# Kernel tuning notes

Hardware: AMD Instinct MI355X
Metric: run time of the kernel (lower is better)

## Reference

```python
import jax, jax.numpy as jnp
import numpy as np
from jax import lax

T, B, NI, NH = 512, 64, 512, 512
SIGMA = 0.01


def _rnn_scan(inputs, W_xh, W_hh, b_h, h0):
    # inputs: [T, B, NI]; precompute input projection as one big GEMM
    xw = jnp.einsum('tbi,ih->tbh', inputs, W_xh)  # [T, B, NH]

    def step(h, x):
        h = jnp.tanh(x + h @ W_hh + b_h)
        return h, h

    hT, hs = lax.scan(step, h0, xw)
    return hs, hT  # hs: [T, B, NH]


def setup_inputs() -> dict:
    key = jax.random.key(0)
    ks = jax.random.split(key, 5)
    inputs = jax.random.normal(ks[0], (T, B, NI), dtype=jnp.float32)
    W_xh_f = jax.random.normal(ks[1], (NI, NH), dtype=jnp.float32) * SIGMA
    W_hh_f = jax.random.normal(ks[2], (NH, NH), dtype=jnp.float32) * SIGMA
    b_h_f = jnp.zeros((NH,), dtype=jnp.float32)
    W_xh_b = jax.random.normal(ks[3], (NI, NH), dtype=jnp.float32) * SIGMA
    W_hh_b = jax.random.normal(ks[4], (NH, NH), dtype=jnp.float32) * SIGMA
    b_h_b = jnp.zeros((NH,), dtype=jnp.float32)
    return {"inputs": inputs, "W_xh_f": W_xh_f, "W_hh_f": W_hh_f, "b_h_f": b_h_f,
            "W_xh_b": W_xh_b, "W_hh_b": W_hh_b, "b_h_b": b_h_b}


def reference(inputs, W_xh_f, W_hh_f, b_h_f, W_xh_b, W_hh_b, b_h_b):
    h0 = jnp.zeros((inputs.shape[1], NH), dtype=inputs.dtype)
    f_outs, f_H = _rnn_scan(inputs, W_xh_f, W_hh_f, b_h_f, h0)
    b_outs_rev, b_H = _rnn_scan(inputs[::-1], W_xh_b, W_hh_b, b_h_b, h0)
    b_outs = b_outs_rev[::-1]  # align backward outputs with forward time order
    outputs = jnp.concatenate([f_outs, b_outs], axis=-1)  # [T, B, 2*NH]
    return outputs, f_H, b_H
```

## Files before the change

kernel.cpp:

```cpp
#include <hip/hip_runtime.h>
#include <hip/hip_bf16.h>


typedef __attribute__((ext_vector_type(8))) short short8;
typedef __attribute__((ext_vector_type(4))) float f32x4;
typedef __attribute__((ext_vector_type(4))) int   i32x4;

static __device__ __forceinline__ float bf2f(unsigned short s) {
  return __builtin_bit_cast(float, ((unsigned int)s) << 16);
}
static __device__ __forceinline__ float tanh_cheap(float x) {
  float t = x * 2.8853900817779268f;
  float e;
  asm("v_exp_f32 %0, %1" : "=v"(e) : "v"(t));
  float den = e + 1.0f;
  float r;
  asm("v_rcp_f32 %0, %1" : "=v"(r) : "v"(den));
  return __builtin_fmaf(-2.0f, r, 1.0f);
}
static __device__ __forceinline__ void lds_barrier() {
  __builtin_amdgcn_sched_barrier(0);
  asm volatile("s_waitcnt lgkmcnt(0)" ::: "memory");
  __builtin_amdgcn_s_barrier();
  __builtin_amdgcn_sched_barrier(0);
}
static __device__ __forceinline__ unsigned int cvt_pk_bf16(float a, float b) {
  unsigned int d;
  asm("v_cvt_pk_bf16_f32 %0, %1, %2" : "=v"(d) : "v"(a), "v"(b));
  return d;
}

__global__ __launch_bounds__(256, 4) void xw_gemm(
    const float* __restrict__ inp,
    const float* __restrict__ Wf,
    const float* __restrict__ Wb,
    const float* __restrict__ bhf,
    const float* __restrict__ bhb,
    unsigned short* __restrict__ xwpf,
    unsigned short* __restrict__ xwpb) {
  __shared__ __align__(16) unsigned short As[64 * 40];
  __shared__ __align__(16) unsigned short Bfs[64 * 40];
  __shared__ __align__(16) unsigned short Bbs[64 * 40];
  const int tid = threadIdx.x;
  const int w = tid >> 6, l = tid & 63;
  const int lr = l & 15, lg = l >> 4;
  const int rbase = blockIdx.x * 64;
  const int nbase = blockIdx.y * 64;

  f32x4 accf[4], accb[4];
#pragma unroll
  for (int tn = 0; tn < 4; ++tn) { accf[tn] = (f32x4){0,0,0,0}; accb[tn] = (f32x4){0,0,0,0}; }

  for (int i = 0; i < 16; ++i) {
    const int k0 = i * 32;
    __syncthreads();
#pragma unroll
    for (int e = 0; e < 2; ++e) {
      int lin4 = tid + e * 256;
      int r = lin4 >> 3, c4 = (lin4 & 7) * 4;
      float4 v = *reinterpret_cast<const float4*>(&inp[(rbase + r) * 512 + k0 + c4]);
      uint2 p;
      p.x = cvt_pk_bf16(v.x, v.y);
      p.y = cvt_pk_bf16(v.z, v.w);
      *reinterpret_cast<uint2*>(&As[r * 40 + c4]) = p;
    }
#pragma unroll
    for (int e = 0; e < 2; ++e) {
      int lin4 = tid + e * 256;
      int r = lin4 >> 4, c4 = (lin4 & 15) * 4;
      float4 vf = *reinterpret_cast<const float4*>(&Wf[(k0 + r) * 512 + nbase + c4]);
      float4 vb = *reinterpret_cast<const float4*>(&Wb[(k0 + r) * 512 + nbase + c4]);
      unsigned int uf0 = cvt_pk_bf16(vf.x, vf.y);
      unsigned int uf1 = cvt_pk_bf16(vf.z, vf.w);
      unsigned int ub0 = cvt_pk_bf16(vb.x, vb.y);
      unsigned int ub1 = cvt_pk_bf16(vb.z, vb.w);
      Bfs[(c4 + 0) * 40 + r] = (unsigned short)uf0;
      Bfs[(c4 + 1) * 40 + r] = (unsigned short)(uf0 >> 16);
      Bfs[(c4 + 2) * 40 + r] = (unsigned short)uf1;
      Bfs[(c4 + 3) * 40 + r] = (unsigned short)(uf1 >> 16);
      Bbs[(c4 + 0) * 40 + r] = (unsigned short)ub0;
      Bbs[(c4 + 1) * 40 + r] = (unsigned short)(ub0 >> 16);
      Bbs[(c4 + 2) * 40 + r] = (unsigned short)ub1;
      Bbs[(c4 + 3) * 40 + r] = (unsigned short)(ub1 >> 16);
    }
    __syncthreads();
    const int ar = w * 16 + lr;
    const int kg = lg * 8;
    short8 a = *reinterpret_cast<const short8*>(&As[ar * 40 + kg]);
#pragma unroll
    for (int tn = 0; tn < 4; ++tn) {
      const int bc = tn * 16 + lr;
      short8 bf = *reinterpret_cast<const short8*>(&Bfs[bc * 40 + kg]);
      short8 bb = *reinterpret_cast<const short8*>(&Bbs[bc * 40 + kg]);
      accf[tn] = __builtin_amdgcn_mfma_f32_16x16x32_bf16(a, bf, accf[tn], 0, 0, 0);
      accb[tn] = __builtin_amdgcn_mfma_f32_16x16x32_bf16(a, bb, accb[tn], 0, 0, 0);
    }
  }
  unsigned long long* pf = reinterpret_cast<unsigned long long*>(xwpf);
  unsigned long long* pb = reinterpret_cast<unsigned long long*>(xwpb);
  const int b64 = (((int)blockIdx.x * 4 + w) * 16 + (int)blockIdx.y * 2) * 128 +
                  (lg * 16 + lr) * 2;
#pragma unroll
  for (int tn = 0; tn < 4; ++tn) {
    const int colb = nbase + tn * 16 + lr;
    const float bfv = bhf[colb], bbv = bhb[colb];
    unsigned long long vf =
        (unsigned long long)cvt_pk_bf16(accf[tn][0] + bfv, accf[tn][1] + bfv)
      | ((unsigned long long)cvt_pk_bf16(accf[tn][2] + bfv, accf[tn][3] + bfv) << 32);
    unsigned long long vb =
        (unsigned long long)cvt_pk_bf16(accb[tn][0] + bbv, accb[tn][1] + bbv)
      | ((unsigned long long)cvt_pk_bf16(accb[tn][2] + bbv, accb[tn][3] + bbv) << 32);
    pf[b64 + (tn >> 1) * 128 + (tn & 1)] = vf;
    pb[b64 + (tn >> 1) * 128 + (tn & 1)] = vb;
  }
}

__global__ __launch_bounds__(1024) void birnn_scan(
    const float* __restrict__ Whf, const float* __restrict__ Whb,
    unsigned short* __restrict__ xwpf, unsigned short* __restrict__ xwpb,
    float* __restrict__ out) {
  const int bid = blockIdx.x;
  const int d  = bid >> 2;
  const int rg = bid & 3;
  const int tid = threadIdx.x;
  const int w = tid >> 6, l = tid & 63;
  const int lr = l & 15, lg = l >> 4;
  const int cbase = w * 32;
  const int rbase = rg * 16;

  const float* Wh = d ? Whb : Whf;
  unsigned short* xwp = d ? xwpb : xwpf;

  __shared__ __align__(16) signed char hq[2][8192];

  const float sW = 127.0f / 0.06f;
  i32x4 wq[2][8];
#pragma unroll
  for (int n = 0; n < 2; ++n) {
    const int col = cbase + n * 16 + lr;
#pragma unroll
    for (int kk = 0; kk < 8; ++kk) {
      i32x4 v;
#pragma unroll
      for (int dw = 0; dw < 4; ++dw) {
        unsigned int pack = 0;
#pragma unroll
        for (int jj = 0; jj < 4; ++jj) {
          const int k = kk * 64 + lg * 16 + dw * 4 + jj;
          float wv = Wh[k * 512 + col] * sW;
          wv = fminf(fmaxf(wv, -127.f), 127.f);
          int q = (int)rintf(wv);
          pack |= ((unsigned int)(q & 0xff)) << (8 * jj);
        }
        v[dw] = (int)pack;
      }
      wq[n][kk] = v;
    }
  }
  const float inv_s = 1.0f / (127.0f * sW);

  short8 xA, xB;
  {
    const int t0 = d ? 511 : 0;
    xA = *reinterpret_cast<const short8*>(
        xwp + (((t0 * 4 + rg) * 16 + w) << 9) + (l << 3));
  }
  {
    const int t1 = d ? 510 : 1;
    xB = *reinterpret_cast<const short8*>(
        xwp + (((t1 * 4 + rg) * 16 + w) << 9) + (l << 3));
  }

  uint4 HP;

#define EPI(N, ACC, U0, U1, FINAL_)                                           \
  {                                                                           \
    float h0_ = tanh_cheap(fmaf((float)(ACC)[0], inv_s, bf2f((unsigned short)X[(N)*4+0]))); \
    float h1_ = tanh_cheap(fmaf((float)(ACC)[1], inv_s, bf2f((unsigned short)X[(N)*4+1]))); \
    float h2_ = tanh_cheap(fmaf((float)(ACC)[2], inv_s, bf2f((unsigned short)X[(N)*4+2]))); \
    float h3_ = tanh_cheap(fmaf((float)(ACC)[3], inv_s, bf2f((unsigned short)X[(N)*4+3]))); \
    signed char* hd_ = &hq[buf_][(w * 2 + (N)) * 256 + lg * 64 + lr];         \
    hd_[0]  = (signed char)(int)rintf(h0_ * 127.f);                           \
    hd_[16] = (signed char)(int)rintf(h1_ * 127.f);                           \
    hd_[32] = (signed char)(int)rintf(h2_ * 127.f);                           \
    hd_[48] = (signed char)(int)rintf(h3_ * 127.f);                           \
    U0 = cvt_pk_bf16(h0_, h1_);                                               \
    U1 = cvt_pk_bf16(h2_, h3_);                                               \
    if (FINAL_) {                                                             \
      float* fo_ = out + 33554432 + d * 32768 + (rbase + lg * 4) * 512 +      \
                   cbase + (N) * 16 + lr;                                     \
      fo_[0] = h0_; fo_[512] = h1_; fo_[1024] = h2_; fo_[1536] = h3_;         \
    }                                                                         \
  }

#define STEP(S, XARG, FINAL_)                                                 \
  do {                                                                        \
    const int s_ = (S);                                                       \
    const int t_ = d ? (511 - s_) : s_;                                       \
    const int buf_ = s_ & 1;                                                  \
    const int pb_ = (s_ - 1) & 1;                                             \
    short8& X = (XARG);                                                       \
    {              \
      const int tp_ = d ? (t_ + 1) : (t_ - 1);                                \
      unsigned short* pw_ = xwp + (((tp_ * 4 + rg) * 16 + w) << 9) + (l << 3);\
      *reinterpret_cast<uint4*>(pw_) = HP;                                    \
    }                                                                         \
    i32x4 acc0 = (i32x4){0,0,0,0}, acc1 = (i32x4){0,0,0,0};                   \
    __builtin_amdgcn_s_setprio(1);                                            \
    {                        \
      const signed char* hb_ = &hq[pb_][lg * 256 + lr * 16];                  \
      i32x4 a0 = *(const i32x4*)(hb_ + 0);                                    \
      i32x4 a1 = *(const i32x4*)(hb_ + 1024);                                 \
      i32x4 a2 = *(const i32x4*)(hb_ + 2048);                                 \
      i32x4 a3 = *(const i32x4*)(hb_ + 3072);                                 \
      acc0 = __builtin_amdgcn_mfma_i32_16x16x64_i8(a0, wq[0][0], acc0, 0, 0, 0); \
      acc1 = __builtin_amdgcn_mfma_i32_16x16x64_i8(a0, wq[1][0], acc1, 0, 0, 0); \
      acc0 = __builtin_amdgcn_mfma_i32_16x16x64_i8(a1, wq[0][1], acc0, 0, 0, 0); \
      acc1 = __builtin_amdgcn_mfma_i32_16x16x64_i8(a1, wq[1][1], acc1, 0, 0, 0); \
      acc0 = __builtin_amdgcn_mfma_i32_16x16x64_i8(a2, wq[0][2], acc0, 0, 0, 0); \
      acc1 = __builtin_amdgcn_mfma_i32_16x16x64_i8(a2, wq[1][2], acc1, 0, 0, 0); \
      acc0 = __builtin_amdgcn_mfma_i32_16x16x64_i8(a3, wq[0][3], acc0, 0, 0, 0); \
      acc1 = __builtin_amdgcn_mfma_i32_16x16x64_i8(a3, wq[1][3], acc1, 0, 0, 0); \
    }                                                                         \
    {                                              \
      const signed char* hb_ = &hq[pb_][(16 + lg) * 256 + lr * 16];           \
      i32x4 a0 = *(const i32x4*)(hb_ + 0);                                    \
      i32x4 a1 = *(const i32x4*)(hb_ + 1024);                                 \
      i32x4 a2 = *(const i32x4*)(hb_ + 2048);                                 \
      i32x4 a3 = *(const i32x4*)(hb_ + 3072);                                 \
      acc0 = __builtin_amdgcn_mfma_i32_16x16x64_i8(a0, wq[0][4], acc0, 0, 0, 0); \
      acc1 = __builtin_amdgcn_mfma_i32_16x16x64_i8(a0, wq[1][4], acc1, 0, 0, 0); \
      acc0 = __builtin_amdgcn_mfma_i32_16x16x64_i8(a1, wq[0][5], acc0, 0, 0, 0); \
      acc1 = __builtin_amdgcn_mfma_i32_16x16x64_i8(a1, wq[1][5], acc1, 0, 0, 0); \
      acc0 = __builtin_amdgcn_mfma_i32_16x16x64_i8(a2, wq[0][6], acc0, 0, 0, 0); \
      acc1 = __builtin_amdgcn_mfma_i32_16x16x64_i8(a2, wq[1][6], acc1, 0, 0, 0); \
      acc0 = __builtin_amdgcn_mfma_i32_16x16x64_i8(a3, wq[0][7], acc0, 0, 0, 0); \
      acc1 = __builtin_amdgcn_mfma_i32_16x16x64_i8(a3, wq[1][7], acc1, 0, 0, 0); \
    }                                                                         \
    __builtin_amdgcn_s_setprio(0);                                            \
    EPI(0, acc0, HP.x, HP.y, FINAL_);                                         \
    EPI(1, acc1, HP.z, HP.w, FINAL_);                                         \
    {                                    \
      const int tp2_ = d ? (t_ - 2) : (t_ + 2);                               \
      X = *reinterpret_cast<const short8*>(                                   \
          xwp + (((tp2_ * 4 + rg) * 16 + w) << 9) + (l << 3));                \
    }                                                                         \
    lds_barrier();                                                            \
  } while (0)

  {
    const int t_ = d ? 511 : 0;
    const int buf_ = 0;
    short8& X = xA;
    i32x4 z_ = (i32x4){0, 0, 0, 0};
    EPI(0, z_, HP.x, HP.y, 0);
    EPI(1, z_, HP.z, HP.w, 0);
    {
      const int tp2_ = d ? (t_ - 2) : (t_ + 2);
      xA = *reinterpret_cast<const short8*>(
          xwp + (((tp2_ * 4 + rg) * 16 + w) << 9) + (l << 3));
    }
    lds_barrier();
  }

  for (int ss = 0; ss < 255; ++ss) {
    STEP(1 + 2 * ss, xB, 0);
    STEP(2 + 2 * ss, xA, 0);
  }
  STEP(511, xB, 1);

  {
    const int tl_ = d ? 0 : 511;
    unsigned short* pw_ = xwp + (((tl_ * 4 + rg) * 16 + w) << 9) + (l << 3);
    *reinterpret_cast<uint4*>(pw_) = HP;
  }
#undef STEP
#undef EPI
}

__global__ __launch_bounds__(1024) void expand_out(
    const unsigned short* __restrict__ xwpf,
    const unsigned short* __restrict__ xwpb,
    float* __restrict__ out) {
  const int g = blockIdx.x * 1024 + threadIdx.x;
  const int flat = g * 4;
  const int row = flat >> 10;
  const int c   = flat & 1023;
  const int t = row >> 6, b = row & 63;
  const int d = c >> 9, col = c & 511;
  const unsigned short* buf = d ? xwpb : xwpf;
  const int lr0 = col & 15;
  const int base = ((t * 4 + (b >> 4)) * 16 + (col >> 5)) * 512 +
                   (((b >> 2) & 3) * 16) * 8 + ((col >> 4) & 1) * 4 + (b & 3);
  float4 v;
  v.x = bf2f(buf[base + (lr0 + 0) * 8]);
  v.y = bf2f(buf[base + (lr0 + 1) * 8]);
  v.z = bf2f(buf[base + (lr0 + 2) * 8]);
  v.w = bf2f(buf[base + (lr0 + 3) * 8]);
  *reinterpret_cast<float4*>(out + flat) = v;
}

extern "C" void kernel_launch(void* const* d_in, const int* in_sizes, int n_in,
                              void* d_out, int out_size, void* d_ws, size_t ws_size,
                              hipStream_t stream) {
  (void)in_sizes; (void)n_in; (void)out_size; (void)ws_size;
  const float* inputs = (const float*)d_in[0];
  const float* W_xh_f = (const float*)d_in[1];
  const float* W_hh_f = (const float*)d_in[2];
  const float* b_h_f  = (const float*)d_in[3];
  const float* W_xh_b = (const float*)d_in[4];
  const float* W_hh_b = (const float*)d_in[5];
  const float* b_h_b  = (const float*)d_in[6];

  unsigned short* xwpf = (unsigned short*)d_ws;
  unsigned short* xwpb = xwpf + 16777216 + 65536;

  dim3 g1(512, 8), b1(256);
  xw_gemm<<<g1, b1, 0, stream>>>(inputs, W_xh_f, W_xh_b, b_h_f, b_h_b, xwpf, xwpb);

  birnn_scan<<<dim3(8), dim3(1024), 0, stream>>>(
      W_hh_f, W_hh_b, xwpf, xwpb, (float*)d_out);

  expand_out<<<dim3(8192), dim3(1024), 0, stream>>>(xwpf, xwpb, (float*)d_out);
}
```

Before: 847.6 us.

## Transpose scan MFMA operands so outputs are row-contiguous, swizzle hidden-state LDS

The recurrent int8 MFMA now takes the weights as the A operand and the hidden state as B, so each lane holds four consecutive hidden columns of one batch row. This lets the epilogue write packed 32-bit int8 hidden-state stores into an XOR-swizzled LDS layout, emit float4 final-state stores, and lets expand_out read one 64-bit word instead of four scattered 16-bit loads. The xw GEMM epilogue stages results through a new LDS tile so its output matches the new per-lane layout. This adds an extra LDS round trip and barriers in the GEMM, and the layout must stay consistent across all three kernels.

```diff
diff --git a/kernel.cpp b/kernel.cpp
--- a/kernel.cpp
+++ b/kernel.cpp
@@ -41,6 +41,7 @@
   __shared__ __align__(16) unsigned short As[64 * 40];
   __shared__ __align__(16) unsigned short Bfs[64 * 40];
   __shared__ __align__(16) unsigned short Bbs[64 * 40];
+  __shared__ __align__(16) unsigned short CT[2][64][68];
   const int tid = threadIdx.x;
   const int w = tid >> 6, l = tid & 63;
   const int lr = l & 15, lg = l >> 4;
@@ -96,22 +97,38 @@
       accb[tn] = __builtin_amdgcn_mfma_f32_16x16x32_bf16(a, bb, accb[tn], 0, 0, 0);
     }
   }
-  unsigned long long* pf = reinterpret_cast<unsigned long long*>(xwpf);
-  unsigned long long* pb = reinterpret_cast<unsigned long long*>(xwpb);
-  const int b64 = (((int)blockIdx.x * 4 + w) * 16 + (int)blockIdx.y * 2) * 128 +
-                  (lg * 16 + lr) * 2;
+  __syncthreads();
 #pragma unroll
   for (int tn = 0; tn < 4; ++tn) {
     const int colb = nbase + tn * 16 + lr;
     const float bfv = bhf[colb], bbv = bhb[colb];
-    unsigned long long vf =
-        (unsigned long long)cvt_pk_bf16(accf[tn][0] + bfv, accf[tn][1] + bfv)
-      | ((unsigned long long)cvt_pk_bf16(accf[tn][2] + bfv, accf[tn][3] + bfv) << 32);
-    unsigned long long vb =
-        (unsigned long long)cvt_pk_bf16(accb[tn][0] + bbv, accb[tn][1] + bbv)
-      | ((unsigned long long)cvt_pk_bf16(accb[tn][2] + bbv, accb[tn][3] + bbv) << 32);
-    pf[b64 + (tn >> 1) * 128 + (tn & 1)] = vf;
-    pb[b64 + (tn >> 1) * 128 + (tn & 1)] = vb;
+    const int gc = tn * 16 + lr;
+#pragma unroll
+    for (int q = 0; q < 4; ++q) {
+      const int gr = w * 16 + lg * 4 + q;
+      CT[0][gr][gc] = (unsigned short)cvt_pk_bf16(accf[tn][q] + bfv, 0.f);
+      CT[1][gr][gc] = (unsigned short)cvt_pk_bf16(accb[tn][q] + bbv, 0.f);
+    }
+  }
+  __syncthreads();
+  unsigned long long* const mats[2] = {
+      reinterpret_cast<unsigned long long*>(xwpf),
+      reinterpret_cast<unsigned long long*>(xwpb)};
+  const int idx0 = tid * 4;
+  const int rgl = idx0 >> 8;
+  const int wl  = (idx0 >> 7) & 1;
+  const int s0  = idx0 & 127;
+#pragma unroll
+  for (int m = 0; m < 2; ++m) {
+    unsigned long long* dst = mats[m] +
+        ((((int)blockIdx.x * 4 + rgl) * 16 + (int)blockIdx.y * 2 + wl) * 128) + s0;
+#pragma unroll
+    for (int e = 0; e < 4; ++e) {
+      const int s64 = s0 + e;
+      const int ls = s64 >> 1, n = s64 & 1;
+      dst[e] = *reinterpret_cast<const unsigned long long*>(
+          &CT[m][rgl * 16 + (ls & 15)][wl * 32 + n * 16 + (ls >> 4) * 4]);
+    }
   }
 }
 
@@ -127,11 +144,14 @@
   const int lr = l & 15, lg = l >> 4;
   const int cbase = w * 32;
   const int rbase = rg * 16;
+  const int sx = lr & 7;
+  const int ro = lr * 512;
 
   const float* Wh = d ? Whb : Whf;
   unsigned short* xwp = d ? xwpb : xwpf;
 
-  __shared__ __align__(16) signed char hq[2][8192];
+  __shared__ __align__(16) signed char hq[2][16][512];
+  signed char* const hqf = &hq[0][0][0];
 
   const float sW = 127.0f / 0.06f;
   i32x4 wq[2][8];
@@ -179,17 +199,20 @@
     float h1_ = tanh_cheap(fmaf((float)(ACC)[1], inv_s, bf2f((unsigned short)X[(N)*4+1]))); \
     float h2_ = tanh_cheap(fmaf((float)(ACC)[2], inv_s, bf2f((unsigned short)X[(N)*4+2]))); \
     float h3_ = tanh_cheap(fmaf((float)(ACC)[3], inv_s, bf2f((unsigned short)X[(N)*4+3]))); \
-    signed char* hd_ = &hq[buf_][(w * 2 + (N)) * 256 + lg * 64 + lr];         \
-    hd_[0]  = (signed char)(int)rintf(h0_ * 127.f);                           \
-    hd_[16] = (signed char)(int)rintf(h1_ * 127.f);                           \
-    hd_[32] = (signed char)(int)rintf(h2_ * 127.f);                           \
-    hd_[48] = (signed char)(int)rintf(h3_ * 127.f);                           \
+    int q0_ = (int)rintf(h0_ * 127.f) & 255;                                  \
+    int q1_ = (int)rintf(h1_ * 127.f) & 255;                                  \
+    int q2_ = (int)rintf(h2_ * 127.f) & 255;                                  \
+    int q3_ = (int)rintf(h3_ * 127.f);                                        \
+    unsigned int pk_ = (unsigned int)q0_ | ((unsigned int)q1_ << 8) |         \
+                       ((unsigned int)q2_ << 16) | ((unsigned int)q3_ << 24); \
+    *reinterpret_cast<unsigned int*>(hqf + buf_ * 8192 + ro +                 \
+        ((((w * 2 + (N)) ^ sx) << 4) + lg * 4)) = pk_;                        \
     U0 = cvt_pk_bf16(h0_, h1_);                                               \
     U1 = cvt_pk_bf16(h2_, h3_);                                               \
     if (FINAL_) {                                                             \
-      float* fo_ = out + 33554432 + d * 32768 + (rbase + lg * 4) * 512 +      \
-                   cbase + (N) * 16 + lr;                                     \
-      fo_[0] = h0_; fo_[512] = h1_; fo_[1024] = h2_; fo_[1536] = h3_;         \
+      float4 fv_; fv_.x = h0_; fv_.y = h1_; fv_.z = h2_; fv_.w = h3_;         \
+      *reinterpret_cast<float4*>(out + 33554432 + d * 32768 +                 \
+          (rbase + lr) * 512 + cbase + (N) * 16 + lg * 4) = fv_;              \
     }                                                                         \
   }
 
@@ -207,35 +230,35 @@
     }                                                                         \
     i32x4 acc0 = (i32x4){0,0,0,0}, acc1 = (i32x4){0,0,0,0};                   \
     __builtin_amdgcn_s_setprio(1);                                            \
-    {                        \
-      const signed char* hb_ = &hq[pb_][lg * 256 + lr * 16];                  \
-      i32x4 a0 = *(const i32x4*)(hb_ + 0);                                    \
-      i32x4 a1 = *(const i32x4*)(hb_ + 1024);                                 \
-      i32x4 a2 = *(const i32x4*)(hb_ + 2048);                                 \
-      i32x4 a3 = *(const i32x4*)(hb_ + 3072);                                 \
-      acc0 = __builtin_amdgcn_mfma_i32_16x16x64_i8(a0, wq[0][0], acc0, 0, 0, 0); \
-      acc1 = __builtin_amdgcn_mfma_i32_16x16x64_i8(a0, wq[1][0], acc1, 0, 0, 0); \
-      acc0 = __builtin_amdgcn_mfma_i32_16x16x64_i8(a1, wq[0][1], acc0, 0, 0, 0); \
-      acc1 = __builtin_amdgcn_mfma_i32_16x16x64_i8(a1, wq[1][1], acc1, 0, 0, 0); \
-      acc0 = __builtin_amdgcn_mfma_i32_16x16x64_i8(a2, wq[0][2], acc0, 0, 0, 0); \
-      acc1 = __builtin_amdgcn_mfma_i32_16x16x64_i8(a2, wq[1][2], acc1, 0, 0, 0); \
-      acc0 = __builtin_amdgcn_mfma_i32_16x16x64_i8(a3, wq[0][3], acc0, 0, 0, 0); \
-      acc1 = __builtin_amdgcn_mfma_i32_16x16x64_i8(a3, wq[1][3], acc1, 0, 0, 0); \
+    {              \
+      const signed char* hb_ = hqf + pb_ * 8192 + ro;                         \
+      i32x4 a0 = *(const i32x4*)(hb_ + ((((0 * 4 + lg) ^ sx) << 4)));         \
+      i32x4 a1 = *(const i32x4*)(hb_ + ((((1 * 4 + lg) ^ sx) << 4)));         \
+      i32x4 a2 = *(const i32x4*)(hb_ + ((((2 * 4 + lg) ^ sx) << 4)));         \
+      i32x4 a3 = *(const i32x4*)(hb_ + ((((3 * 4 + lg) ^ sx) << 4)));         \
+      acc0 = __builtin_amdgcn_mfma_i32_16x16x64_i8(wq[0][0], a0, acc0, 0, 0, 0); \
+      acc1 = __builtin_amdgcn_mfma_i32_16x16x64_i8(wq[1][0], a0, acc1, 0, 0, 0); \
+      acc0 = __builtin_amdgcn_mfma_i32_16x16x64_i8(wq[0][1], a1, acc0, 0, 0, 0); \
+      acc1 = __builtin_amdgcn_mfma_i32_16x16x64_i8(wq[1][1], a1, acc1, 0, 0, 0); \
+      acc0 = __builtin_amdgcn_mfma_i32_16x16x64_i8(wq[0][2], a2, acc0, 0, 0, 0); \
+      acc1 = __builtin_amdgcn_mfma_i32_16x16x64_i8(wq[1][2], a2, acc1, 0, 0, 0); \
+      acc0 = __builtin_amdgcn_mfma_i32_16x16x64_i8(wq[0][3], a3, acc0, 0, 0, 0); \
+      acc1 = __builtin_amdgcn_mfma_i32_16x16x64_i8(wq[1][3], a3, acc1, 0, 0, 0); \
     }                                                                         \
     {                                              \
-      const signed char* hb_ = &hq[pb_][(16 + lg) * 256 + lr * 16];           \
-      i32x4 a0 = *(const i32x4*)(hb_ + 0);                                    \
-      i32x4 a1 = *(const i32x4*)(hb_ + 1024);                                 \
-      i32x4 a2 = *(const i32x4*)(hb_ + 2048);                                 \
-      i32x4 a3 = *(const i32x4*)(hb_ + 3072);                                 \
-      acc0 = __builtin_amdgcn_mfma_i32_16x16x64_i8(a0, wq[0][4], acc0, 0, 0, 0); \
-      acc1 = __builtin_amdgcn_mfma_i32_16x16x64_i8(a0, wq[1][4], acc1, 0, 0, 0); \
-      acc0 = __builtin_amdgcn_mfma_i32_16x16x64_i8(a1, wq[0][5], acc0, 0, 0, 0); \
-      acc1 = __builtin_amdgcn_mfma_i32_16x16x64_i8(a1, wq[1][5], acc1, 0, 0, 0); \
-      acc0 = __builtin_amdgcn_mfma_i32_16x16x64_i8(a2, wq[0][6], acc0, 0, 0, 0); \
-      acc1 = __builtin_amdgcn_mfma_i32_16x16x64_i8(a2, wq[1][6], acc1, 0, 0, 0); \
-      acc0 = __builtin_amdgcn_mfma_i32_16x16x64_i8(a3, wq[0][7], acc0, 0, 0, 0); \
-      acc1 = __builtin_amdgcn_mfma_i32_16x16x64_i8(a3, wq[1][7], acc1, 0, 0, 0); \
+      const signed char* hb_ = hqf + pb_ * 8192 + ro;                         \
+      i32x4 a0 = *(const i32x4*)(hb_ + ((((4 * 4 + lg) ^ sx) << 4)));         \
+      i32x4 a1 = *(const i32x4*)(hb_ + ((((5 * 4 + lg) ^ sx) << 4)));         \
+      i32x4 a2 = *(const i32x4*)(hb_ + ((((6 * 4 + lg) ^ sx) << 4)));         \
+      i32x4 a3 = *(const i32x4*)(hb_ + ((((7 * 4 + lg) ^ sx) << 4)));         \
+      acc0 = __builtin_amdgcn_mfma_i32_16x16x64_i8(wq[0][4], a0, acc0, 0, 0, 0); \
+      acc1 = __builtin_amdgcn_mfma_i32_16x16x64_i8(wq[1][4], a0, acc1, 0, 0, 0); \
+      acc0 = __builtin_amdgcn_mfma_i32_16x16x64_i8(wq[0][5], a1, acc0, 0, 0, 0); \
+      acc1 = __builtin_amdgcn_mfma_i32_16x16x64_i8(wq[1][5], a1, acc1, 0, 0, 0); \
+      acc0 = __builtin_amdgcn_mfma_i32_16x16x64_i8(wq[0][6], a2, acc0, 0, 0, 0); \
+      acc1 = __builtin_amdgcn_mfma_i32_16x16x64_i8(wq[1][6], a2, acc1, 0, 0, 0); \
+      acc0 = __builtin_amdgcn_mfma_i32_16x16x64_i8(wq[0][7], a3, acc0, 0, 0, 0); \
+      acc1 = __builtin_amdgcn_mfma_i32_16x16x64_i8(wq[1][7], a3, acc1, 0, 0, 0); \
     }                                                                         \
     __builtin_amdgcn_s_setprio(0);                                            \
     EPI(0, acc0, HP.x, HP.y, FINAL_);                                         \
@@ -288,15 +311,16 @@
   const int c   = flat & 1023;
   const int t = row >> 6, b = row & 63;
   const int d = c >> 9, col = c & 511;
-  const unsigned short* buf = d ? xwpb : xwpf;
-  const int lr0 = col & 15;
-  const int base = ((t * 4 + (b >> 4)) * 16 + (col >> 5)) * 512 +
-                   (((b >> 2) & 3) * 16) * 8 + ((col >> 4) & 1) * 4 + (b & 3);
+  const unsigned long long* buf = reinterpret_cast<const unsigned long long*>(
+      d ? xwpb : xwpf);
+  const int lidx = ((col >> 2) & 3) * 16 + (b & 15);
+  const int chunk = (t * 4 + (b >> 4)) * 16 + (col >> 5);
+  unsigned long long hv = buf[chunk * 128 + lidx * 2 + ((col >> 4) & 1)];
   float4 v;
-  v.x = bf2f(buf[base + (lr0 + 0) * 8]);
-  v.y = bf2f(buf[base + (lr0 + 1) * 8]);
-  v.z = bf2f(buf[base + (lr0 + 2) * 8]);
-  v.w = bf2f(buf[base + (lr0 + 3) * 8]);
+  v.x = bf2f((unsigned short)hv);
+  v.y = bf2f((unsigned short)(hv >> 16));
+  v.z = bf2f((unsigned short)(hv >> 32));
+  v.w = bf2f((unsigned short)(hv >> 48));
   *reinterpret_cast<float4*>(out + flat) = v;
 }
 
```

After: 851.8 us. About the same (+0.5%).
